# Kernel tuning notes

Hardware: AMD Instinct MI355X
Metric: run time of the kernel (lower is better)

Reference implementation:

```python
import jax, jax.numpy as jnp
import numpy as np

NODES = 81
NODE_DIM = 2
IN_DIM = NODES * NODE_DIM  # 162
D = 256
H = 16
HD = D // H
DFF = 2048
T, B, E = 1024, 8, 648


def _layernorm(x, w, b, eps=1e-5):
    m = x.mean(-1, keepdims=True)
    v = x.var(-1, keepdims=True)
    return (x - m) / jnp.sqrt(v + eps) * w + b


def setup_inputs() -> dict:
    key = jax.random.key(0)
    ks = jax.random.split(key, 12)
    s = 0.02
    W = lambda k, shape: jax.random.normal(k, shape, jnp.float32) * s
    return {
        "src": jax.random.normal(ks[0], (T, B, IN_DIM), jnp.float32),
        "edge_index": jax.random.randint(ks[1], (2, E), 0, NODES),
        "gcn_w": W(ks[2], (NODE_DIM, NODE_DIM)),
        "gcn_b": jnp.zeros((NODE_DIM,), jnp.float32),
        "fc_w": W(ks[3], (IN_DIM, D)),
        "fc_b": jnp.zeros((D,), jnp.float32),
        "wq": W(ks[4], (D, D)), "bq": jnp.zeros((D,), jnp.float32),
        "wk": W(ks[5], (D, D)), "bk": jnp.zeros((D,), jnp.float32),
        "wv": W(ks[6], (D, D)), "bv": jnp.zeros((D,), jnp.float32),
        "wo": W(ks[7], (D, D)), "bo": jnp.zeros((D,), jnp.float32),
        "ln1_w": jnp.ones((D,), jnp.float32), "ln1_b": jnp.zeros((D,), jnp.float32),
        "ffn_w1": W(ks[8], (D, DFF)), "ffn_b1": jnp.zeros((DFF,), jnp.float32),
        "ffn_w2": W(ks[9], (DFF, D)), "ffn_b2": jnp.zeros((D,), jnp.float32),
        "ln2_w": jnp.ones((D,), jnp.float32), "ln2_b": jnp.zeros((D,), jnp.float32),
        "dec_w": W(ks[10], (D, IN_DIM)), "dec_b": jnp.zeros((IN_DIM,), jnp.float32),
    }


def reference(src, edge_index, gcn_w, gcn_b, fc_w, fc_b, wq, bq, wk, bk, wv, bv,
              wo, bo, ln1_w, ln1_b, ffn_w1, ffn_b1, ffn_w2, ffn_b2, ln2_w, ln2_b,
              dec_w, dec_b):
    t, b, _ = src.shape
    # ---- batched GCNConv(2,2): all T*B tiny graphs share one adjacency ----
    # src[t,b] = [in_flow(81), out_flow(81)] -> node features [81, 2]
    xg = jnp.swapaxes(src.reshape(t, b, NODE_DIM, NODES), -1, -2)  # [T,B,81,2]
    row, col = edge_index[0], edge_index[1]
    A = jnp.zeros((NODES, NODES), src.dtype).at[col, row].add(1.0)
    A = A + jnp.eye(NODES, dtype=src.dtype)          # add self-loops
    deg = A.sum(1)
    dinv = jnp.where(deg > 0, 1.0 / jnp.sqrt(deg), 0.0)
    A_hat = dinv[:, None] * A * dinv[None, :]        # D^-1/2 (A+I) D^-1/2
    hg = jnp.einsum('ij,tbjc->tbic', A_hat, xg @ gcn_w) + gcn_b  # [T,B,81,2]
    # gcn_output.transpose(0,1).view(-1): channel-major flatten
    src2 = jnp.swapaxes(hg, -1, -2).reshape(t, b, IN_DIM)
    # ---- fc + positional encoding ----
    x = src2 @ fc_w + fc_b  # [T,B,D]
    pos = jnp.arange(t, dtype=jnp.float32)[:, None]
    div = jnp.exp(jnp.arange(0, D, 2, dtype=jnp.float32) * (-np.log(10000.0) / D))
    pe = jnp.zeros((t, D), x.dtype).at[:, 0::2].set(jnp.sin(pos * div))
    pe = pe.at[:, 1::2].set(jnp.cos(pos * div))
    x = x + pe[:, None, :]
    # ---- TransformerEncoderLayer (post-norm, relu, causal mask, eval) ----
    q = (x @ wq + bq).reshape(t, b, H, HD)
    k = (x @ wk + bk).reshape(t, b, H, HD)
    v = (x @ wv + bv).reshape(t, b, H, HD)
    scores = jnp.einsum('tbhd,sbhd->bhts', q, k) / jnp.sqrt(jnp.asarray(HD, x.dtype))
    causal = jnp.tril(jnp.ones((t, t), bool))
    scores = jnp.where(causal, scores, jnp.finfo(x.dtype).min)
    attn = jax.nn.softmax(scores, axis=-1)
    ctx = jnp.einsum('bhts,sbhd->tbhd', attn, v).reshape(t, b, D) @ wo + bo
    x = _layernorm(x + ctx, ln1_w, ln1_b)
    ff = jax.nn.relu(x @ ffn_w1 + ffn_b1) @ ffn_w2 + ffn_b2
    x = _layernorm(x + ff, ln2_w, ln2_b)
    return x @ dec_w + dec_b  # [T,B,162]
```

## Files before the change

kernel.cpp:

```cpp
#include <hip/hip_runtime.h>
#include <math.h>

#define T_    1024
#define B_    8
#define D_    256
#define H_    16
#define HD_   16
#define DFF_  2048
#define NODES_ 81
#define INDIM_ 162
#define E_    648
#define M_    (T_*B_)

typedef __bf16 bf16x8 __attribute__((ext_vector_type(8)));
typedef float  f32x4  __attribute__((ext_vector_type(4)));
typedef unsigned short ushort_t;
typedef unsigned int   uint_t;

union bfpack { bf16x8 v; uint_t u[4]; };

__device__ __forceinline__ ushort_t f2bf(float f) {
    union { float f; uint_t u; } c; c.f = f;
    uint_t u = c.u;
    uint_t r = u + 0x7fffu + ((u >> 16) & 1u);
    return (ushort_t)(r >> 16);
}

__device__ __forceinline__ uint_t fbits(float f) {
    union { float f; uint_t u; } c; c.f = f;
    return c.u;
}

__device__ __forceinline__ float truncbf(float f) {
    union { uint_t u; float f; } c; c.u = fbits(f) & 0xffff0000u;
    return c.f;
}

__device__ __forceinline__ bf16x8 zero8() {
    bf16x8 v;
#pragma unroll
    for (int e = 0; e < 8; e++) v[e] = (__bf16)0.0f;
    return v;
}

__device__ __forceinline__ void gload_lds16(const void* g, void* l) {
    __builtin_amdgcn_global_load_lds(
        (const __attribute__((address_space(1))) void*)g,
        (__attribute__((address_space(3))) void*)l, 16, 0, 0);
}

__device__ __forceinline__ void trans_tile(
        const float* __restrict__ in, ushort_t* __restrict__ out,
        float (*tile)[33], int K, int N, int Kp, int bx, int by) {
    int k0 = bx * 32, n0 = by * 32;
    int tx = threadIdx.x & 31, ty = threadIdx.x >> 5;
#pragma unroll
    for (int i = 0; i < 4; i++) {
        int r = k0 + ty + i * 8, c = n0 + tx;
        tile[ty + i * 8][tx] = (r < K && c < N) ? in[(size_t)r * N + c] : 0.f;
    }
    __syncthreads();
#pragma unroll
    for (int i = 0; i < 4; i++) {
        int r = n0 + ty + i * 8, c = k0 + tx;
        out[(size_t)r * Kp + c] = f2bf(tile[tx][ty + i * 8]);
    }
}

__global__ __launch_bounds__(256) void prep_all(
        const int* __restrict__ edge, const float* __restrict__ gcn_w,
        const float* __restrict__ gcn_b, const float* __restrict__ fc_w,
        const float* __restrict__ fc_b, const float* __restrict__ src,
        const float* __restrict__ wq, const float* __restrict__ wk,
        const float* __restrict__ wv, const float* __restrict__ wo,
        const float* __restrict__ dec_w, const float* __restrict__ w1,
        const float* __restrict__ w2,
        const float* __restrict__ bq, const float* __restrict__ bk,
        const float* __restrict__ bv,
        ushort_t* __restrict__ weffT, float* __restrict__ beff,
        ushort_t* __restrict__ srcb,
        ushort_t* __restrict__ wqkvT, ushort_t* __restrict__ woT,
        ushort_t* __restrict__ dwT, ushort_t* __restrict__ w1T,
        ushort_t* __restrict__ w2T, float* __restrict__ qkvbias) {
    __shared__ float A[NODES_ * NODES_];
    __shared__ float dinv[NODES_];
    __shared__ float tile[32][33];
    int bid = blockIdx.x;
    int tid = threadIdx.x;
    if (bid < 82) {
        for (int i = tid; i < NODES_ * NODES_; i += 256) A[i] = 0.f;
        __syncthreads();
        for (int e = tid; e < E_; e += 256) {
            int r = edge[e];
            int c = edge[E_ + e];
            atomicAdd(&A[c * NODES_ + r], 1.0f);
        }
        __syncthreads();
        if (tid < NODES_) A[tid * NODES_ + tid] += 1.0f;
        __syncthreads();
        if (tid < NODES_) {
            float s = 0.f;
            for (int k = 0; k < NODES_; k++) s += A[tid * NODES_ + k];
            dinv[tid] = (s > 0.f) ? rsqrtf(s) : 0.f;
        }
        __syncthreads();
        int d = tid, j = bid;
        if (j < NODES_) {
            float s0 = 0.f, s1 = 0.f;
            for (int i = 0; i < NODES_; i++) {
                float a = dinv[i] * A[i * NODES_ + j] * dinv[j];
                s0 += a * fc_w[(0 * NODES_ + i) * D_ + d];
                s1 += a * fc_w[(1 * NODES_ + i) * D_ + d];
            }
            weffT[d * 192 + j]          = f2bf(gcn_w[0] * s0 + gcn_w[1] * s1);
            weffT[d * 192 + NODES_ + j] = f2bf(gcn_w[2] * s0 + gcn_w[3] * s1);
        } else {
            float t0 = 0.f, t1 = 0.f;
            for (int i = 0; i < NODES_; i++) {
                t0 += fc_w[(0 * NODES_ + i) * D_ + d];
                t1 += fc_w[(1 * NODES_ + i) * D_ + d];
            }
            beff[d] = fc_b[d] + gcn_b[0] * t0 + gcn_b[1] * t1;
            for (int c = INDIM_; c < 192; c++) weffT[d * 192 + c] = 0;
        }
    } else if (bid < 1426) {
        int l = bid - 82;
        if (l < 64)        trans_tile(wq,    wqkvT,          tile, D_,   D_,     D_,   l & 7,  l >> 3);
        else if (l < 128)  trans_tile(wk,    wqkvT + 65536,  tile, D_,   D_,     D_,   (l-64) & 7,  (l-64) >> 3);
        else if (l < 192)  trans_tile(wv,    wqkvT + 131072, tile, D_,   D_,     D_,   (l-128) & 7, (l-128) >> 3);
        else if (l < 256)  trans_tile(wo,    woT,            tile, D_,   D_,     D_,   (l-192) & 7, (l-192) >> 3);
        else if (l < 320)  trans_tile(dec_w, dwT,            tile, D_,   INDIM_, D_,   (l-256) & 7, (l-256) >> 3);
        else if (l < 832)  trans_tile(w1,    w1T,            tile, D_,   DFF_,   D_,   (l-320) & 7, (l-320) >> 3);
        else               trans_tile(w2,    w2T,            tile, DFF_, D_,     DFF_, (l-832) & 63, (l-832) >> 6);
    } else if (bid == 1426) {
#pragma unroll
        for (int k = 0; k < 3; k++) {
            int i = k * 256 + tid;
            qkvbias[i] = (i < 256) ? bq[i] : ((i < 512) ? bk[i - 256] : bv[i - 512]);
        }
    } else {
        int r = bid - 1427;
        if (tid < 192)
            srcb[(size_t)r * 192 + tid] =
                (tid < INDIM_) ? f2bf(src[(size_t)r * INDIM_ + tid]) : (ushort_t)0;
    }
}

enum { EP_PE = 0, EP_QKV = 1, EP_RELU = 3, EP_DEC = 4 };

template <int EPI, int TM>
__global__ __launch_bounds__(256) void gemm_bf16(
        const ushort_t* __restrict__ A, const ushort_t* __restrict__ BT,
        const float* __restrict__ bias, float* __restrict__ Cf,
        ushort_t* __restrict__ Cb, int M, int N, int K) {
    __shared__ ushort_t sA[TM * 64];
    __shared__ ushort_t sB[128 * 64];
    int tid = threadIdx.x;
    int w = tid >> 6, lane = tid & 63;
    int cc = lane & 15, q = lane >> 4;
    int bm = blockIdx.y * TM, bn = blockIdx.x * 128;

    int srow = (lane >> 3);
    int sslot = lane & 7;

    const int NJ = (TM == 128) ? 4 : 2;
    int mbase = (TM == 128) ? ((w >> 1) * 64) : 0;
    int nbase = (TM == 128) ? ((w & 1) * 64) : (w * 32);

    f32x4 acc[4][NJ];
#pragma unroll
    for (int i = 0; i < 4; i++)
#pragma unroll
        for (int j = 0; j < NJ; j++)
#pragma unroll
            for (int e = 0; e < 4; e++) acc[i][j][e] = 0.f;

    for (int k0 = 0; k0 < K; k0 += 64) {
        if (TM == 128) {
#pragma unroll
            for (int i = 0; i < 4; i++) {
                int r = w * 32 + i * 8 + srow;
                const ushort_t* ga = A + (size_t)(bm + r) * K + k0 + ((sslot ^ (r & 7)) * 8);
                gload_lds16(ga, &sA[(w * 32 + i * 8) * 64]);
            }
        } else {
#pragma unroll
            for (int i = 0; i < 2; i++) {
                int r = w * 16 + i * 8 + srow;
                const ushort_t* ga = A + (size_t)(bm + r) * K + k0 + ((sslot ^ (r & 7)) * 8);
                gload_lds16(ga, &sA[(w * 16 + i * 8) * 64]);
            }
        }
#pragma unroll
        for (int i = 0; i < 4; i++) {
            int r = w * 32 + i * 8 + srow;
            const ushort_t* gb = BT + (size_t)(bn + r) * K + k0 + ((sslot ^ (r & 7)) * 8);
            gload_lds16(gb, &sB[(w * 32 + i * 8) * 64]);
        }
        __syncthreads();
#pragma unroll
        for (int ks = 0; ks < 2; ks++) {
            bf16x8 af[4], bfr[NJ];
#pragma unroll
            for (int i = 0; i < 4; i++) {
                int m = mbase + i * 16 + cc;
                int off = m * 64 + (((ks * 4 + q) ^ (cc & 7)) * 8);
                af[i] = *(const bf16x8*)&sA[off];
            }
#pragma unroll
            for (int j = 0; j < NJ; j++) {
                int n = nbase + j * 16 + cc;
                int off = n * 64 + (((ks * 4 + q) ^ (cc & 7)) * 8);
                bfr[j] = *(const bf16x8*)&sB[off];
            }
#pragma unroll
            for (int i = 0; i < 4; i++)
#pragma unroll
                for (int j = 0; j < NJ; j++)
                    acc[i][j] = __builtin_amdgcn_mfma_f32_16x16x32_bf16(af[i], bfr[j], acc[i][j], 0, 0, 0);
        }
        __syncthreads();
    }

#pragma unroll
    for (int i = 0; i < 4; i++) {
#pragma unroll
        for (int j = 0; j < NJ; j++) {
            int col = bn + nbase + j * 16 + cc;
            float bv;
            if (EPI == EP_DEC) bv = (col < INDIM_) ? bias[col] : 0.f;
            else bv = bias[col];
#pragma unroll
            for (int reg = 0; reg < 4; reg++) {
                int row = bm + mbase + i * 16 + q * 4 + reg;
                float v = acc[i][j][reg] + bv;
                if (EPI == EP_PE) {
                    int t = row >> 3;
                    float freq = __expf((float)(col & ~1) * (-9.210340371976184f / 256.f));
                    float ang = (float)t * freq;
                    v += (col & 1) ? __cosf(ang) : __sinf(ang);
                    Cf[(size_t)row * N + col] = v;
                    Cb[(size_t)row * N + col] = f2bf(v);
                } else if (EPI == EP_QKV) {
                    int t = row >> 3, b = row & 7;
                    int nn = col & 255, which = col >> 8;
                    int h = nn >> 4, hd = nn & 15;
                    Cb[(size_t)which * 2097152 +
                       ((size_t)((b * H_ + h) * T_ + t)) * HD_ + hd] = f2bf(v);
                } else if (EPI == EP_RELU) {
                    v = fmaxf(v, 0.f);
                    Cb[(size_t)row * N + col] = f2bf(v);
                } else if (EPI == EP_DEC) {
                    if (col < INDIM_) Cf[(size_t)row * INDIM_ + col] = v;
                }
            }
        }
    }
}

template <int K, bool WF>
__global__ __launch_bounds__(256) void gemm_ln(
        const ushort_t* __restrict__ A, const ushort_t* __restrict__ BT,
        const float* __restrict__ bias, const float* __restrict__ X,
        const float* __restrict__ lnw, const float* __restrict__ lnb,
        float* __restrict__ Yf, ushort_t* __restrict__ Yb) {
    __shared__ ushort_t sA[32 * 64];
    __shared__ ushort_t sB[256 * 64];
    __shared__ float redS[32 * 4];
    __shared__ float redQ[32 * 4];
    int tid = threadIdx.x;
    int w = tid >> 6, lane = tid & 63;
    int cc = lane & 15, q = lane >> 4;
    int bm = blockIdx.x * 32;
    int srow = lane >> 3, sslot = lane & 7;

    f32x4 acc[2][4];
#pragma unroll
    for (int i = 0; i < 2; i++)
#pragma unroll
        for (int j = 0; j < 4; j++)
#pragma unroll
            for (int e = 0; e < 4; e++) acc[i][j][e] = 0.f;

    for (int k0 = 0; k0 < K; k0 += 64) {
        {
            int r = w * 8 + srow;
            const ushort_t* ga = A + (size_t)(bm + r) * K + k0 + ((sslot ^ (r & 7)) * 8);
            gload_lds16(ga, &sA[(w * 8) * 64]);
        }
#pragma unroll
        for (int i = 0; i < 8; i++) {
            int r = i * 32 + w * 8 + srow;
            const ushort_t* gb = BT + (size_t)r * K + k0 + ((sslot ^ (r & 7)) * 8);
            gload_lds16(gb, &sB[(i * 32 + w * 8) * 64]);
        }
        __syncthreads();
#pragma unroll
        for (int ks = 0; ks < 2; ks++) {
            bf16x8 af[2], bfr[4];
#pragma unroll
            for (int i = 0; i < 2; i++) {
                int m = i * 16 + cc;
                af[i] = *(const bf16x8*)&sA[m * 64 + (((ks * 4 + q) ^ (cc & 7)) * 8)];
            }
#pragma unroll
            for (int j = 0; j < 4; j++) {
                int n = w * 64 + j * 16 + cc;
                bfr[j] = *(const bf16x8*)&sB[n * 64 + (((ks * 4 + q) ^ (cc & 7)) * 8)];
            }
#pragma unroll
            for (int i = 0; i < 2; i++)
#pragma unroll
                for (int j = 0; j < 4; j++)
                    acc[i][j] = __builtin_amdgcn_mfma_f32_16x16x32_bf16(af[i], bfr[j], acc[i][j], 0, 0, 0);
        }
        __syncthreads();
    }

    float ls[2][4], lq[2][4];
#pragma unroll
    for (int i = 0; i < 2; i++)
#pragma unroll
        for (int reg = 0; reg < 4; reg++) { ls[i][reg] = 0.f; lq[i][reg] = 0.f; }
#pragma unroll
    for (int i = 0; i < 2; i++) {
#pragma unroll
        for (int j = 0; j < 4; j++) {
            int col = w * 64 + j * 16 + cc;
            float bv = bias[col];
#pragma unroll
            for (int reg = 0; reg < 4; reg++) {
                int row = bm + i * 16 + q * 4 + reg;
                float t = acc[i][j][reg] + bv + X[(size_t)row * D_ + col];
                acc[i][j][reg] = t;
                ls[i][reg] += t;
                lq[i][reg] += t * t;
            }
        }
    }
#pragma unroll
    for (int m = 1; m < 16; m <<= 1) {
#pragma unroll
        for (int i = 0; i < 2; i++)
#pragma unroll
            for (int reg = 0; reg < 4; reg++) {
                ls[i][reg] += __shfl_xor(ls[i][reg], m);
                lq[i][reg] += __shfl_xor(lq[i][reg], m);
            }
    }
    if (cc == 0) {
#pragma unroll
        for (int i = 0; i < 2; i++)
#pragma unroll
            for (int reg = 0; reg < 4; reg++) {
                int r = i * 16 + q * 4 + reg;
                redS[r * 4 + w] = ls[i][reg];
                redQ[r * 4 + w] = lq[i][reg];
            }
    }
    __syncthreads();
#pragma unroll
    for (int i = 0; i < 2; i++) {
#pragma unroll
        for (int reg = 0; reg < 4; reg++) {
            int r = i * 16 + q * 4 + reg;
            float S  = redS[r * 4 + 0] + redS[r * 4 + 1] + redS[r * 4 + 2] + redS[r * 4 + 3];
            float Q2 = redQ[r * 4 + 0] + redQ[r * 4 + 1] + redQ[r * 4 + 2] + redQ[r * 4 + 3];
            float mean = S * (1.f / 256.f);
            float var  = Q2 * (1.f / 256.f) - mean * mean;
            float rstd = rsqrtf(var + 1e-5f);
            int row = bm + r;
#pragma unroll
            for (int j = 0; j < 4; j++) {
                int col = w * 64 + j * 16 + cc;
                float y = (acc[i][j][reg] - mean) * rstd * lnw[col] + lnb[col];
                if (WF) Yf[(size_t)row * D_ + col] = y;
                Yb[(size_t)row * D_ + col] = f2bf(y);
            }
        }
    }
}

__global__ __launch_bounds__(256) void attn_mfma(
        const ushort_t* __restrict__ Qb, const ushort_t* __restrict__ Kb,
        const ushort_t* __restrict__ Vb, float* __restrict__ partO,
        float* __restrict__ partL) {
    const int qc_of[20] = {0,1,2,2,3,3,4,4,4,5,5,5,6,6,6,6,7,7,7,7};
    const int kp_of[20] = {0,0,0,1,0,1,0,1,2,0,1,2,0,1,2,3,0,1,2,3};
    int slot = blockIdx.x;
    int qc = qc_of[slot], kp = kp_of[slot];
    int bh = blockIdx.y;
    int tid = threadIdx.x;
    int w = tid >> 6, lane = tid & 63;
    int cc = lane & 15, q = lane >> 4;
    int qb0 = qc * 128;
    int kbeg = kp * 4;
    int kend = 2 * (qc + 1);
    if (kend > kbeg + 4) kend = kbeg + 4;

    __shared__ ushort_t VTs[2][16 * 72];

    const ushort_t* Qp = Qb + (size_t)bh * (T_ * HD_);
    const ushort_t* Kp = Kb + (size_t)bh * (T_ * HD_);
    const ushort_t* Vp = Vb + (size_t)bh * (T_ * HD_);

    bf16x8 qf[2];
#pragma unroll
    for (int i = 0; i < 2; i++) {
        if (q < 2)
            qf[i] = *(const bf16x8*)&Qp[(size_t)(qb0 + w * 32 + i * 16 + cc) * HD_ + q * 8];
        else
            qf[i] = zero8();
    }

    f32x4 ot[2];
    float lacc[2] = {0.f, 0.f};
#pragma unroll
    for (int i = 0; i < 2; i++)
#pragma unroll
        for (int e = 0; e < 4; e++) ot[i][e] = 0.f;

    int qmaxw = qb0 + w * 32 + 31;

    for (int kb = kbeg; kb < kend; kb++) {
        ushort_t* vbuf = VTs[kb & 1];
        if (tid < 128) {
            int r = tid >> 1, half = tid & 1;
            bf16x8 vv = *(const bf16x8*)&Vp[(size_t)(kb * 64 + r) * HD_ + half * 8];
#pragma unroll
            for (int e = 0; e < 8; e++)
                vbuf[(half * 8 + e) * 72 + r] = ((const ushort_t*)&vv)[e];
        }
        __syncthreads();
        if (kb * 64 > qmaxw) continue;

        f32x4 s[2][4];
#pragma unroll
        for (int j = 0; j < 4; j++) {
            bf16x8 kf;
            if (q < 2)
                kf = *(const bf16x8*)&Kp[(size_t)(kb * 64 + j * 16 + cc) * HD_ + q * 8];
            else
                kf = zero8();
#pragma unroll
            for (int i = 0; i < 2; i++) {
                f32x4 z;
#pragma unroll
                for (int e = 0; e < 4; e++) z[e] = 0.f;
                s[i][j] = __builtin_amdgcn_mfma_f32_16x16x32_bf16(kf, qf[i], z, 0, 0, 0);
            }
        }

#pragma unroll
        for (int j = 0; j < 4; j++) {
            bfpack af;
            const uint_t* vt = (const uint_t*)&vbuf[cc * 72 + j * 16 + q * 4];
            af.u[0] = vt[0]; af.u[1] = vt[1]; af.u[2] = 0u; af.u[3] = 0u;
            int key0 = kb * 64 + j * 16 + q * 4;
#pragma unroll
            for (int i = 0; i < 2; i++) {
                int qrow = qb0 + w * 32 + i * 16 + cc;
                float p0 = __expf(s[i][j][0] * 0.25f);
                float p1 = __expf(s[i][j][1] * 0.25f);
                float p2 = __expf(s[i][j][2] * 0.25f);
                float p3 = __expf(s[i][j][3] * 0.25f);
                if (key0 + 0 > qrow) p0 = 0.f;
                if (key0 + 1 > qrow) p1 = 0.f;
                if (key0 + 2 > qrow) p2 = 0.f;
                if (key0 + 3 > qrow) p3 = 0.f;
                bfpack pf;
                pf.u[0] = (fbits(p0) >> 16) | (fbits(p1) & 0xffff0000u);
                pf.u[1] = (fbits(p2) >> 16) | (fbits(p3) & 0xffff0000u);
                pf.u[2] = 0u; pf.u[3] = 0u;
                ot[i] = __builtin_amdgcn_mfma_f32_16x16x32_bf16(af.v, pf.v, ot[i], 0, 0, 0);
                lacc[i] += truncbf(p0) + truncbf(p1) + truncbf(p2) + truncbf(p3);
            }
        }
    }

    int base = (bh * 20 + slot) * 128;
#pragma unroll
    for (int i = 0; i < 2; i++) {
        float l0 = lacc[i];
        l0 += __shfl_xor(l0, 16);
        l0 += __shfl_xor(l0, 32);
        int row = w * 32 + i * 16 + cc;
        *(f32x4*)&partO[((size_t)(base + row)) * 16 + q * 4] = ot[i];
        if (q == 0) partL[base + row] = l0;
    }
}

__global__ __launch_bounds__(256) void attn_reduce(
        const float* __restrict__ partO, const float* __restrict__ partL,
        ushort_t* __restrict__ ctxb) {
    const int cum[9] = {0, 1, 2, 4, 6, 9, 12, 16, 20};
    int qc = blockIdx.x, bh = blockIdx.y;
    int row = threadIdx.x >> 1, dh = threadIdx.x & 1;
    int p0 = cum[qc], p1 = cum[qc + 1];
    float o[8];
#pragma unroll
    for (int e = 0; e < 8; e++) o[e] = 0.f;
    float l = 0.f;
    for (int p = p0; p < p1; p++) {
        size_t base = ((size_t)bh * 20 + p) * 128 + row;
        const float4 a = *(const float4*)&partO[base * 16 + dh * 8];
        const float4 b4 = *(const float4*)&partO[base * 16 + dh * 8 + 4];
        o[0] += a.x; o[1] += a.y; o[2] += a.z; o[3] += a.w;
        o[4] += b4.x; o[5] += b4.y; o[6] += b4.z; o[7] += b4.w;
        l += partL[base];
    }
    float inv = 1.f / l;
    int t = qc * 128 + row, b = bh >> 4, h = bh & 15;
    ushort_t* op = ctxb + ((size_t)t * B_ + b) * D_ + h * HD_ + dh * 8;
    ushort4 u0, u1;
    u0.x = f2bf(o[0] * inv); u0.y = f2bf(o[1] * inv);
    u0.z = f2bf(o[2] * inv); u0.w = f2bf(o[3] * inv);
    u1.x = f2bf(o[4] * inv); u1.y = f2bf(o[5] * inv);
    u1.z = f2bf(o[6] * inv); u1.w = f2bf(o[7] * inv);
    *(ushort4*)&op[0] = u0;
    *(ushort4*)&op[4] = u1;
}

extern "C" void kernel_launch(void* const* d_in, const int* in_sizes, int n_in,
                              void* d_out, int out_size, void* d_ws, size_t ws_size,
                              hipStream_t stream) {
    (void)in_sizes; (void)n_in; (void)out_size; (void)ws_size;
    const float* src     = (const float*)d_in[0];
    const int*   edge    = (const int*)d_in[1];
    const float* gcn_w   = (const float*)d_in[2];
    const float* gcn_b   = (const float*)d_in[3];
    const float* fc_w    = (const float*)d_in[4];
    const float* fc_b    = (const float*)d_in[5];
    const float* wq      = (const float*)d_in[6];
    const float* bq      = (const float*)d_in[7];
    const float* wk      = (const float*)d_in[8];
    const float* bk      = (const float*)d_in[9];
    const float* wv      = (const float*)d_in[10];
    const float* bv      = (const float*)d_in[11];
    const float* wo      = (const float*)d_in[12];
    const float* bo      = (const float*)d_in[13];
    const float* ln1_w   = (const float*)d_in[14];
    const float* ln1_b   = (const float*)d_in[15];
    const float* ffn_w1  = (const float*)d_in[16];
    const float* ffn_b1  = (const float*)d_in[17];
    const float* ffn_w2  = (const float*)d_in[18];
    const float* ffn_b2  = (const float*)d_in[19];
    const float* ln2_w   = (const float*)d_in[20];
    const float* ln2_b   = (const float*)d_in[21];
    const float* dec_w   = (const float*)d_in[22];
    const float* dec_b   = (const float*)d_in[23];
    float* out = (float*)d_out;

    float* ws = (float*)d_ws;
    float* beff    = ws;
    float* qkvbias = ws + 256;
    float* x0      = ws + 1024;
    float* x1      = x0 + 2097152;
    ushort_t* ub   = (ushort_t*)(ws + 4195328);
    ushort_t* srcb = ub;
    ushort_t* x0b  = ub + 1572864;
    ushort_t* x1b  = x0b + 2097152;
    ushort_t* x2b  = x1b + 2097152;
    ushort_t* ctxb = x2b + 2097152;
    ushort_t* hb   = ctxb + 2097152;
    ushort_t* qkvb = hb + 16777216;
    ushort_t* weffT= qkvb + 6291456;
    ushort_t* wqkvT= weffT + 49152;
    ushort_t* woT  = wqkvT + 196608;
    ushort_t* w1T  = woT + 65536;
    ushort_t* w2T  = w1T + 524288;
    ushort_t* dwT  = w2T + 524288;
    float* partO = (float*)hb;
    float* partL = partO + 5242880;

    prep_all<<<9619, 256, 0, stream>>>(edge, gcn_w, gcn_b, fc_w, fc_b, src,
                                       wq, wk, wv, wo, dec_w, ffn_w1, ffn_w2,
                                       bq, bk, bv, weffT, beff, srcb,
                                       wqkvT, woT, dwT, w1T, w2T, qkvbias);

    gemm_bf16<EP_PE, 64><<<dim3(2, 128), 256, 0, stream>>>(srcb, weffT, beff, x0, x0b, M_, D_, 192);
    gemm_bf16<EP_QKV, 64><<<dim3(6, 128), 256, 0, stream>>>(x0b, wqkvT, qkvbias, nullptr, qkvb, M_, 768, D_);
    attn_mfma<<<dim3(20, 128), 256, 0, stream>>>(qkvb, qkvb + 2097152, qkvb + 4194304, partO, partL);
    attn_reduce<<<dim3(8, 128), 256, 0, stream>>>(partO, partL, ctxb);
    gemm_ln<256, true><<<256, 256, 0, stream>>>(ctxb, woT, bo, x0, ln1_w, ln1_b, x1, x1b);
    gemm_bf16<EP_RELU, 128><<<dim3(16, 64), 256, 0, stream>>>(x1b, w1T, ffn_b1, nullptr, hb, M_, DFF_, D_);
    gemm_ln<2048, false><<<256, 256, 0, stream>>>(hb, w2T, ffn_b2, x1, ln2_w, ln2_b, nullptr, x2b);
    gemm_bf16<EP_DEC, 64><<<dim3(2, 128), 256, 0, stream>>>(x2b, dwT, dec_b, out, nullptr, M_, D_, D_);
}
```

Measured before the change: 246.0 us.

## Replace split-K attention plus reduce kernel with paired causal-chunk blocks

The attention work is no longer split across 20 key-partition slots per head with a separate reduction kernel. Each block now handles a pair of query chunks (qc and 7-qc) so causal work is balanced, and it normalizes and writes bf16 context directly. This removes the partial-output write/read traffic and one kernel launch, but cuts the grid from 2560 to 512 blocks and lengthens each block's serial loop, which may reduce occupancy and latency hiding.

Measured after the change: 246.5 us. About the same (+0.2%).

```diff
diff --git a/kernel.cpp b/kernel.cpp
--- a/kernel.cpp
+++ b/kernel.cpp
@@ -383,142 +383,115 @@
 
 __global__ __launch_bounds__(256) void attn_mfma(
         const ushort_t* __restrict__ Qb, const ushort_t* __restrict__ Kb,
-        const ushort_t* __restrict__ Vb, float* __restrict__ partO,
-        float* __restrict__ partL) {
-    const int qc_of[20] = {0,1,2,2,3,3,4,4,4,5,5,5,6,6,6,6,7,7,7,7};
-    const int kp_of[20] = {0,0,0,1,0,1,0,1,2,0,1,2,0,1,2,3,0,1,2,3};
-    int slot = blockIdx.x;
-    int qc = qc_of[slot], kp = kp_of[slot];
+        const ushort_t* __restrict__ Vb, ushort_t* __restrict__ ctxb) {
+    int pair = blockIdx.x;
     int bh = blockIdx.y;
     int tid = threadIdx.x;
     int w = tid >> 6, lane = tid & 63;
     int cc = lane & 15, q = lane >> 4;
-    int qb0 = qc * 128;
-    int kbeg = kp * 4;
-    int kend = 2 * (qc + 1);
-    if (kend > kbeg + 4) kend = kbeg + 4;
 
     __shared__ ushort_t VTs[2][16 * 72];
 
     const ushort_t* Qp = Qb + (size_t)bh * (T_ * HD_);
     const ushort_t* Kp = Kb + (size_t)bh * (T_ * HD_);
     const ushort_t* Vp = Vb + (size_t)bh * (T_ * HD_);
-
-    bf16x8 qf[2];
-#pragma unroll
-    for (int i = 0; i < 2; i++) {
-        if (q < 2)
-            qf[i] = *(const bf16x8*)&Qp[(size_t)(qb0 + w * 32 + i * 16 + cc) * HD_ + q * 8];
-        else
-            qf[i] = zero8();
-    }
-
-    f32x4 ot[2];
-    float lacc[2] = {0.f, 0.f};
-#pragma unroll
-    for (int i = 0; i < 2; i++)
-#pragma unroll
-        for (int e = 0; e < 4; e++) ot[i][e] = 0.f;
-
-    int qmaxw = qb0 + w * 32 + 31;
-
-    for (int kb = kbeg; kb < kend; kb++) {
-        ushort_t* vbuf = VTs[kb & 1];
-        if (tid < 128) {
-            int r = tid >> 1, half = tid & 1;
-            bf16x8 vv = *(const bf16x8*)&Vp[(size_t)(kb * 64 + r) * HD_ + half * 8];
-#pragma unroll
-            for (int e = 0; e < 8; e++)
-                vbuf[(half * 8 + e) * 72 + r] = ((const ushort_t*)&vv)[e];
-        }
-        __syncthreads();
-        if (kb * 64 > qmaxw) continue;
-
-        f32x4 s[2][4];
-#pragma unroll
-        for (int j = 0; j < 4; j++) {
-            bf16x8 kf;
+    int b = bh >> 4, h = bh & 15;
+
+    int tt = 0;
+#pragma unroll
+    for (int half = 0; half < 2; half++) {
+        int qc = (half == 0) ? pair : (7 - pair);
+        int qb0 = qc * 128;
+        int ntiles = 2 * (qc + 1);
+        int qmaxw = qb0 + w * 32 + 31;
+
+        bf16x8 qf[2];
+#pragma unroll
+        for (int i = 0; i < 2; i++) {
             if (q < 2)
-                kf = *(const bf16x8*)&Kp[(size_t)(kb * 64 + j * 16 + cc) * HD_ + q * 8];
+                qf[i] = *(const bf16x8*)&Qp[(size_t)(qb0 + w * 32 + i * 16 + cc) * HD_ + q * 8];
             else
-                kf = zero8();
-#pragma unroll
-            for (int i = 0; i < 2; i++) {
-                f32x4 z;
-#pragma unroll
-                for (int e = 0; e < 4; e++) z[e] = 0.f;
-                s[i][j] = __builtin_amdgcn_mfma_f32_16x16x32_bf16(kf, qf[i], z, 0, 0, 0);
-            }
-        }
-
-#pragma unroll
-        for (int j = 0; j < 4; j++) {
-            bfpack af;
-            const uint_t* vt = (const uint_t*)&vbuf[cc * 72 + j * 16 + q * 4];
-            af.u[0] = vt[0]; af.u[1] = vt[1]; af.u[2] = 0u; af.u[3] = 0u;
-            int key0 = kb * 64 + j * 16 + q * 4;
-#pragma unroll
-            for (int i = 0; i < 2; i++) {
-                int qrow = qb0 + w * 32 + i * 16 + cc;
-                float p0 = __expf(s[i][j][0] * 0.25f);
-                float p1 = __expf(s[i][j][1] * 0.25f);
-                float p2 = __expf(s[i][j][2] * 0.25f);
-                float p3 = __expf(s[i][j][3] * 0.25f);
-                if (key0 + 0 > qrow) p0 = 0.f;
-                if (key0 + 1 > qrow) p1 = 0.f;
-                if (key0 + 2 > qrow) p2 = 0.f;
-                if (key0 + 3 > qrow) p3 = 0.f;
-                bfpack pf;
-                pf.u[0] = (fbits(p0) >> 16) | (fbits(p1) & 0xffff0000u);
-                pf.u[1] = (fbits(p2) >> 16) | (fbits(p3) & 0xffff0000u);
-                pf.u[2] = 0u; pf.u[3] = 0u;
-                ot[i] = __builtin_amdgcn_mfma_f32_16x16x32_bf16(af.v, pf.v, ot[i], 0, 0, 0);
-                lacc[i] += truncbf(p0) + truncbf(p1) + truncbf(p2) + truncbf(p3);
-            }
-        }
-    }
-
-    int base = (bh * 20 + slot) * 128;
-#pragma unroll
-    for (int i = 0; i < 2; i++) {
-        float l0 = lacc[i];
-        l0 += __shfl_xor(l0, 16);
-        l0 += __shfl_xor(l0, 32);
-        int row = w * 32 + i * 16 + cc;
-        *(f32x4*)&partO[((size_t)(base + row)) * 16 + q * 4] = ot[i];
-        if (q == 0) partL[base + row] = l0;
-    }
-}
-
-__global__ __launch_bounds__(256) void attn_reduce(
-        const float* __restrict__ partO, const float* __restrict__ partL,
-        ushort_t* __restrict__ ctxb) {
-    const int cum[9] = {0, 1, 2, 4, 6, 9, 12, 16, 20};
-    int qc = blockIdx.x, bh = blockIdx.y;
-    int row = threadIdx.x >> 1, dh = threadIdx.x & 1;
-    int p0 = cum[qc], p1 = cum[qc + 1];
-    float o[8];
-#pragma unroll
-    for (int e = 0; e < 8; e++) o[e] = 0.f;
-    float l = 0.f;
-    for (int p = p0; p < p1; p++) {
-        size_t base = ((size_t)bh * 20 + p) * 128 + row;
-        const float4 a = *(const float4*)&partO[base * 16 + dh * 8];
-        const float4 b4 = *(const float4*)&partO[base * 16 + dh * 8 + 4];
-        o[0] += a.x; o[1] += a.y; o[2] += a.z; o[3] += a.w;
-        o[4] += b4.x; o[5] += b4.y; o[6] += b4.z; o[7] += b4.w;
-        l += partL[base];
-    }
-    float inv = 1.f / l;
-    int t = qc * 128 + row, b = bh >> 4, h = bh & 15;
-    ushort_t* op = ctxb + ((size_t)t * B_ + b) * D_ + h * HD_ + dh * 8;
-    ushort4 u0, u1;
-    u0.x = f2bf(o[0] * inv); u0.y = f2bf(o[1] * inv);
-    u0.z = f2bf(o[2] * inv); u0.w = f2bf(o[3] * inv);
-    u1.x = f2bf(o[4] * inv); u1.y = f2bf(o[5] * inv);
-    u1.z = f2bf(o[6] * inv); u1.w = f2bf(o[7] * inv);
-    *(ushort4*)&op[0] = u0;
-    *(ushort4*)&op[4] = u1;
+                qf[i] = zero8();
+        }
+
+        f32x4 ot[2];
+        float lacc[2] = {0.f, 0.f};
+#pragma unroll
+        for (int i = 0; i < 2; i++)
+#pragma unroll
+            for (int e = 0; e < 4; e++) ot[i][e] = 0.f;
+
+        for (int kb = 0; kb < ntiles; kb++, tt++) {
+            ushort_t* vbuf = VTs[tt & 1];
+            if (tid < 128) {
+                int r = tid >> 1, hf = tid & 1;
+                bf16x8 vv = *(const bf16x8*)&Vp[(size_t)(kb * 64 + r) * HD_ + hf * 8];
+#pragma unroll
+                for (int e = 0; e < 8; e++)
+                    vbuf[(hf * 8 + e) * 72 + r] = ((const ushort_t*)&vv)[e];
+            }
+            __syncthreads();
+            if (kb * 64 > qmaxw) continue;
+
+            f32x4 s[2][4];
+#pragma unroll
+            for (int j = 0; j < 4; j++) {
+                bf16x8 kf;
+                if (q < 2)
+                    kf = *(const bf16x8*)&Kp[(size_t)(kb * 64 + j * 16 + cc) * HD_ + q * 8];
+                else
+                    kf = zero8();
+#pragma unroll
+                for (int i = 0; i < 2; i++) {
+                    f32x4 z;
+#pragma unroll
+                    for (int e = 0; e < 4; e++) z[e] = 0.f;
+                    s[i][j] = __builtin_amdgcn_mfma_f32_16x16x32_bf16(kf, qf[i], z, 0, 0, 0);
+                }
+            }
+
+#pragma unroll
+            for (int j = 0; j < 4; j++) {
+                bfpack af;
+                const uint_t* vt = (const uint_t*)&vbuf[cc * 72 + j * 16 + q * 4];
+                af.u[0] = vt[0]; af.u[1] = vt[1]; af.u[2] = 0u; af.u[3] = 0u;
+                int key0 = kb * 64 + j * 16 + q * 4;
+#pragma unroll
+                for (int i = 0; i < 2; i++) {
+                    int qrow = qb0 + w * 32 + i * 16 + cc;
+                    float p0 = __expf(s[i][j][0] * 0.25f);
+                    float p1 = __expf(s[i][j][1] * 0.25f);
+                    float p2 = __expf(s[i][j][2] * 0.25f);
+                    float p3 = __expf(s[i][j][3] * 0.25f);
+                    if (key0 + 0 > qrow) p0 = 0.f;
+                    if (key0 + 1 > qrow) p1 = 0.f;
+                    if (key0 + 2 > qrow) p2 = 0.f;
+                    if (key0 + 3 > qrow) p3 = 0.f;
+                    bfpack pf;
+                    pf.u[0] = (fbits(p0) >> 16) | (fbits(p1) & 0xffff0000u);
+                    pf.u[1] = (fbits(p2) >> 16) | (fbits(p3) & 0xffff0000u);
+                    pf.u[2] = 0u; pf.u[3] = 0u;
+                    ot[i] = __builtin_amdgcn_mfma_f32_16x16x32_bf16(af.v, pf.v, ot[i], 0, 0, 0);
+                    lacc[i] += truncbf(p0) + truncbf(p1) + truncbf(p2) + truncbf(p3);
+                }
+            }
+        }
+
+#pragma unroll
+        for (int i = 0; i < 2; i++) {
+            float l0 = lacc[i];
+            l0 += __shfl_xor(l0, 16);
+            l0 += __shfl_xor(l0, 32);
+            float linv = 1.f / l0;
+            int t = qb0 + w * 32 + i * 16 + cc;
+            ushort4 ov;
+            ov.x = f2bf(ot[i][0] * linv);
+            ov.y = f2bf(ot[i][1] * linv);
+            ov.z = f2bf(ot[i][2] * linv);
+            ov.w = f2bf(ot[i][3] * linv);
+            *(ushort4*)&ctxb[((size_t)t * B_ + b) * D_ + h * HD_ + q * 4] = ov;
+        }
+    }
 }
 
 extern "C" void kernel_launch(void* const* d_in, const int* in_sizes, int n_in,
@@ -570,8 +543,6 @@
     ushort_t* w1T  = woT + 65536;
     ushort_t* w2T  = w1T + 524288;
     ushort_t* dwT  = w2T + 524288;
-    float* partO = (float*)hb;
-    float* partL = partO + 5242880;
 
     prep_all<<<9619, 256, 0, stream>>>(edge, gcn_w, gcn_b, fc_w, fc_b, src,
                                        wq, wk, wv, wo, dec_w, ffn_w1, ffn_w2,
@@ -580,8 +551,7 @@
 
     gemm_bf16<EP_PE, 64><<<dim3(2, 128), 256, 0, stream>>>(srcb, weffT, beff, x0, x0b, M_, D_, 192);
     gemm_bf16<EP_QKV, 64><<<dim3(6, 128), 256, 0, stream>>>(x0b, wqkvT, qkvbias, nullptr, qkvb, M_, 768, D_);
-    attn_mfma<<<dim3(20, 128), 256, 0, stream>>>(qkvb, qkvb + 2097152, qkvb + 4194304, partO, partL);
-    attn_reduce<<<dim3(8, 128), 256, 0, stream>>>(partO, partL, ctxb);
+    attn_mfma<<<dim3(4, 128), 256, 0, stream>>>(qkvb, qkvb + 2097152, qkvb + 4194304, ctxb);
     gemm_ln<256, true><<<256, 256, 0, stream>>>(ctxb, woT, bo, x0, ln1_w, ln1_b, x1, x1b);
     gemm_bf16<EP_RELU, 128><<<dim3(16, 64), 256, 0, stream>>>(x1b, w1T, ffn_b1, nullptr, hb, M_, DFF_, D_);
     gemm_ln<2048, false><<<256, 256, 0, stream>>>(hb, w2T, ffn_b2, x1, ln2_w, ln2_b, nullptr, x2b);
```
